# Optimization experiments

Measured on AMD Instinct MI355X. Metric: run time of the kernel, lower is better.

The kernel has to match this reference:

```python
import jax, jax.numpy as jnp
import numpy as np

S, B, E, H, V, L = 512, 64, 512, 768, 32000, 32
PAD_WORD, PAD_LABEL = 1, 0
PAD_BIAS = 10000.0


def _linear_init(key, fin, fout):
    # matches torch nn.Linear default U(-1/sqrt(fin), 1/sqrt(fin))
    kw, kb = jax.random.split(key)
    s = 1.0 / np.sqrt(fin)
    W = jax.random.uniform(kw, (fin, fout), minval=-s, maxval=s, dtype=jnp.float32)
    b = jax.random.uniform(kb, (fout,), minval=-s, maxval=s, dtype=jnp.float32)
    return W, b


def setup_inputs() -> dict:
    key = jax.random.key(0)
    ks = jax.random.split(key, 9)
    tokens = jax.random.randint(ks[0], (S, B), 0, V, dtype=jnp.int32)
    tags = jax.random.randint(ks[1], (S, B), 0, L, dtype=jnp.int32)
    embedding = jax.random.normal(ks[2], (V, E), dtype=jnp.float32)
    # gate order along the 4H axis: r, f, g, o (matches the 8 separate Linears, stacked)
    Wi_f, bi_f = _linear_init(ks[3], E, 4 * H)
    Wh_f, bh_f = _linear_init(ks[4], H, 4 * H)
    Wi_b, bi_b = _linear_init(ks[5], E, 4 * H)
    Wh_b, bh_b = _linear_init(ks[6], H, 4 * H)
    Wout, bout = _linear_init(ks[7], 2 * H, L)
    return {"tokens": tokens, "tags": tags, "embedding": embedding,
            "Wi_f": Wi_f, "bi_f": bi_f, "Wh_f": Wh_f, "bh_f": bh_f,
            "Wi_b": Wi_b, "bi_b": bi_b, "Wh_b": Wh_b, "bh_b": bh_b,
            "Wout": Wout, "bout": bout}


def _forward(tokens, embedding, Wi_f, bi_f, Wh_f, bh_f, Wi_b, bi_b, Wh_b, bh_b, Wout, bout):
    emb = embedding[tokens]                      # [S,B,E]
    b = tokens.shape[1]
    h = emb.shape[-1] * 0 + Wh_f.shape[0]
    # ---- forward direction: true LSTM-style recurrence ----
    xf = jnp.einsum('sbe,eg->sbg', emb, Wi_f) + bi_f   # [S,B,4H] precomputed input gates

    def step_f(carry, x):
        hid, c = carry
        g = x + hid @ Wh_f + bh_f
        r, f, gg, o = jnp.split(g, 4, axis=-1)
        c = jax.nn.sigmoid(f) * c + jax.nn.sigmoid(r) * jnp.tanh(gg)
        hid = jax.nn.sigmoid(o) * jnp.tanh(c)
        return (hid, c), hid

    z = jnp.zeros((b, h), dtype=emb.dtype)
    (hT, _), hs_f = jax.lax.scan(step_f, (z, z), xf)   # hs_f: [S,B,H]

    # ---- backward direction: source never updates `hidden`, so the hidden
    # projection uses the CONSTANT final forward hidden hT at every step.
    gb = jnp.einsum('sbe,eg->sbg', emb, Wi_b) + bi_b + hT @ Wh_b + bh_b  # [S,B,4H]
    r2, f2, g2, o2 = jnp.split(gb, 4, axis=-1)
    r2 = jax.nn.sigmoid(r2); f2 = jax.nn.sigmoid(f2)
    g2 = jnp.tanh(g2);       o2 = jax.nn.sigmoid(o2)

    def step_b(c2, gates):
        r, f, g, o = gates
        c2 = f * c2 + r * g
        return c2, o * jnp.tanh(c2)

    _, hs_b = jax.lax.scan(step_b, z, (r2, f2, g2, o2), reverse=True)  # [S,B,H], original order

    outputs = jnp.concatenate([hs_f, hs_b], axis=-1)   # [S,B,2H]
    out = outputs @ Wout + bout                        # [S,B,L]
    pad_mask = (tokens == PAD_WORD).astype(out.dtype)
    out = out.at[:, :, PAD_LABEL].add(pad_mask * PAD_BIAS)
    return out


def reference(tokens, tags, embedding, Wi_f, bi_f, Wh_f, bh_f, Wi_b, bi_b, Wh_b, bh_b, Wout, bout):
    del tags  # unused in forward, kept for signature fidelity
    return _forward(tokens, embedding, Wi_f, bi_f, Wh_f, bh_f, Wi_b, bi_b, Wh_b, bh_b, Wout, bout)
```

## Files before the change

kernel.cpp:

```cpp
#include <hip/hip_runtime.h>
#include <hip/hip_bf16.h>
#include <stdint.h>

typedef __attribute__((ext_vector_type(8))) short bf16x8;
typedef __attribute__((ext_vector_type(4))) float f32x4;
typedef __attribute__((ext_vector_type(4))) unsigned int u32x4;
typedef unsigned long long ull_t;

#define S_LEN 512
#define B_DIM 64
#define E_DIM 512
#define H_DIM 768
#define G4    3072
#define H2    1536
#define M_ROWS 32768
#define CHUNK 128
#define CM    8192
#define SLW   24
#define WPS   8
#define WPR   256
#define RWRD  4096
#define PSTR  16384
#define KRES  640
#define KREG  4
#define WROW  648

__device__ __forceinline__ float sigmf_(float x) { return 1.0f / (1.0f + __expf(-x)); }
__device__ __forceinline__ float tanhf2(float x) {
  x = fminf(fmaxf(x, -20.0f), 20.0f);
  float e = __expf(2.0f * x);
  return (e - 1.0f) / (e + 1.0f);
}
__device__ __forceinline__ float bfu(unsigned short u) { return __uint_as_float((unsigned)u << 16); }
__device__ __forceinline__ unsigned short packbf(float a) {
  __hip_bfloat16 t = __float2bfloat16(a);
  unsigned short b;
  __builtin_memcpy(&b, &t, 2);
  return b;
}

__global__ __launch_bounds__(256) void k_gather(const int* __restrict__ tokens,
                                                const float* __restrict__ emb,
                                                __hip_bfloat16* __restrict__ out) {
  const int t = blockIdx.x * 256 + threadIdx.x;
  const int e0 = t * 8;
  const int row = e0 >> 9;
  const int k = e0 & 511;
  const int tok = tokens[row];
  const float4* p = (const float4*)(emb + (size_t)tok * E_DIM + k);
  const float4 v0 = p[0], v1 = p[1];
  __align__(16) __hip_bfloat16 tmp[8];
  tmp[0] = __float2bfloat16(v0.x); tmp[1] = __float2bfloat16(v0.y);
  tmp[2] = __float2bfloat16(v0.z); tmp[3] = __float2bfloat16(v0.w);
  tmp[4] = __float2bfloat16(v1.x); tmp[5] = __float2bfloat16(v1.y);
  tmp[6] = __float2bfloat16(v1.z); tmp[7] = __float2bfloat16(v1.w);
  *(bf16x8*)(out + (size_t)t * 8) = *(const bf16x8*)tmp;
}

__global__ __launch_bounds__(256) void k_transpose_cast(const float* __restrict__ src,
                                                        __hip_bfloat16* __restrict__ dst,
                                                        int Rs, int Cs) {
  __shared__ float tile[32][33];
  const int tx = threadIdx.x & 31, ty = threadIdx.x >> 5;
  const int c0 = blockIdx.x * 32, r0 = blockIdx.y * 32;
  #pragma unroll
  for (int i = ty; i < 32; i += 8)
    tile[i][tx] = src[(size_t)(r0 + i) * Cs + c0 + tx];
  __syncthreads();
  #pragma unroll
  for (int i = ty; i < 32; i += 8)
    dst[(size_t)(c0 + i) * Rs + r0 + tx] = __float2bfloat16(tile[tx][i]);
}

__global__ __launch_bounds__(256) void k_bias(const float* __restrict__ bi,
                                              const float* __restrict__ bh,
                                              float* __restrict__ bias) {
  const int n = blockIdx.x * 256 + threadIdx.x;
  bias[n] = bi[n] + bh[n];
}

__global__ __launch_bounds__(256) void k_gemm_x(const __hip_bfloat16* __restrict__ A,
                                                const __hip_bfloat16* __restrict__ BT,
                                                const float* __restrict__ bias,
                                                __hip_bfloat16* __restrict__ C) {
  __shared__ __align__(16) __hip_bfloat16 As[128][40];
  __shared__ __align__(16) __hip_bfloat16 Bs[128][40];
  const int tid = threadIdx.x;
  const int wave = tid >> 6, lane = tid & 63;
  const int q = lane >> 4, lr = lane & 15;
  const int wm = (wave >> 1) * 64, wn = (wave & 1) * 64;
  const int m0 = blockIdx.y * 128, n0 = blockIdx.x * 128;
  const int srow = tid >> 2, skseg = (tid & 3) * 8;

  f32x4 acc[4][4];
  #pragma unroll
  for (int i = 0; i < 4; ++i)
    #pragma unroll
    for (int j = 0; j < 4; ++j) { f32x4 z = {0.f, 0.f, 0.f, 0.f}; acc[i][j] = z; }

  for (int kt = 0; kt < 16; ++kt) {
    __syncthreads();
    const int kbase = kt * 32 + skseg;
    *(bf16x8*)&As[srow][skseg]      = *(const bf16x8*)(A + (size_t)(m0 + srow) * E_DIM + kbase);
    *(bf16x8*)&As[srow + 64][skseg] = *(const bf16x8*)(A + (size_t)(m0 + srow + 64) * E_DIM + kbase);
    *(bf16x8*)&Bs[srow][skseg]      = *(const bf16x8*)(BT + (size_t)(n0 + srow) * E_DIM + kbase);
    *(bf16x8*)&Bs[srow + 64][skseg] = *(const bf16x8*)(BT + (size_t)(n0 + srow + 64) * E_DIM + kbase);
    __syncthreads();
    bf16x8 af[4], bfr[4];
    #pragma unroll
    for (int mt = 0; mt < 4; ++mt) af[mt] = *(const bf16x8*)&As[wm + mt * 16 + lr][q * 8];
    #pragma unroll
    for (int nt = 0; nt < 4; ++nt) bfr[nt] = *(const bf16x8*)&Bs[wn + nt * 16 + lr][q * 8];
    #pragma unroll
    for (int mt = 0; mt < 4; ++mt)
      #pragma unroll
      for (int nt = 0; nt < 4; ++nt)
        acc[mt][nt] = __builtin_amdgcn_mfma_f32_16x16x32_bf16(af[mt], bfr[nt], acc[mt][nt], 0, 0, 0);
  }
  #pragma unroll
  for (int mt = 0; mt < 4; ++mt) {
    #pragma unroll
    for (int nt = 0; nt < 4; ++nt) {
      const int col = n0 + wn + nt * 16 + lr;
      const float bv = bias[col];
      #pragma unroll
      for (int i = 0; i < 4; ++i) {
        const int row = m0 + wm + mt * 16 + q * 4 + i;
        C[(size_t)row * G4 + col] = __float2bfloat16(acc[mt][nt][i] + bv);
      }
    }
  }
}

__global__ __launch_bounds__(256, 1) void k_fwd_scan(const __hip_bfloat16* __restrict__ X,
                                                     const __hip_bfloat16* __restrict__ WhTf,
                                                     ull_t* __restrict__ hbuf,
                                                     __hip_bfloat16* __restrict__ Hs,
                                                     float* __restrict__ cstate,
                                                     float* __restrict__ hT,
                                                     int chunk) {
  const int bx = blockIdx.x;
  const int group = bx >> 5;
  const int slice = bx & 31;
  const int r0 = group * 16;
  const int j0 = slice * SLW;
  const int tid = threadIdx.x;
  const int w = tid >> 6;
  const int lane = tid & 63;
  const int q = lane >> 4, lr = lane & 15;
  const int base = chunk * CHUNK;

  const int prow = tid >> 4;
  const int pw   = tid & 15;

  const int row  = tid >> 3;
  const int wloc = tid & 7;
  const int col0 = 3 * wloc;

  __shared__ __align__(16) unsigned short wlds[4 * SLW * WROW];
  __shared__ __align__(16) unsigned short h_stage[16][776];
  __shared__ float g_lds[4][16][26];

  for (int c = tid; c < 96 * (KRES / 8); c += 256) {
    const int r = c / (KRES / 8), k8 = c % (KRES / 8);
    const int gate = r / SLW, n = r % SLW;
    const float4 v = *(const float4*)(WhTf + (size_t)(gate * H_DIM + j0 + n) * H_DIM + k8 * 8);
    *(float4*)(wlds + (size_t)r * WROW + k8 * 8) = v;
  }

  const int wn0 = lr;
  const int wn1 = 16 + (lr & 7);
  bf16x8 wr0[KREG], wr1[KREG];
  #pragma unroll
  for (int kk = 0; kk < KREG; ++kk) {
    const int ko = KRES + kk * 32 + q * 8;
    wr0[kk] = *(const bf16x8*)(WhTf + (size_t)(w * H_DIM + j0 + wn0) * H_DIM + ko);
    wr1[kk] = *(const bf16x8*)(WhTf + (size_t)(w * H_DIM + j0 + wn1) * H_DIM + ko);
  }

  float cr[3] = {0.f, 0.f, 0.f};
  if (tid < 128) {
    const float* cs = cstate + (size_t)(r0 + row) * H_DIM + j0 + col0;
    cr[0] = cs[0]; cr[1] = cs[1]; cr[2] = cs[2];
  }

  const unsigned skipbit = ((pw >> 2) == (slice & 3)) ? (1u << (slice >> 2)) : 0u;

  __syncthreads();

  for (int s = 0; s < CHUNK; ++s) {
    const int gs = base + s;

    unsigned short xs[4][3];
    if (tid < 128) {
      const unsigned short* xp = (const unsigned short*)(X + ((size_t)s * B_DIM + r0 + row) * G4 + j0 + col0);
      #pragma unroll
      for (int g = 0; g < 4; ++g)
        #pragma unroll
        for (int j = 0; j < 3; ++j) xs[g][j] = xp[g * H_DIM + j];
    }

    const ull_t* hc = hbuf + ((size_t)(gs & 1)) * PSTR + (size_t)group * RWRD
                    + (size_t)prow * WPR + 2 * pw;
    u32x4 d0 = {0,0,0,0}, d1 = {0,0,0,0}, d2 = {0,0,0,0}, d3 = {0,0,0,0};
    u32x4 d4 = {0,0,0,0}, d5 = {0,0,0,0}, d6 = {0,0,0,0}, d7 = {0,0,0,0};
    const unsigned pollmask = (s == 0) ? 0xFFu : (0xFFu ^ skipbit);
    {
      const unsigned e16 = (unsigned)(unsigned short)gs;
      unsigned need = pollmask;
      long guard = 0;
      for (;;) {
#define POLL_LD(i, dv) \
        if (need & (1u << (i))) \
          asm volatile("global_load_dwordx4 %0, %1, off sc0 sc1" \
                       : "=v"(dv) : "v"(hc + 32 * (i)) : "memory");
        POLL_LD(0, d0) POLL_LD(1, d1) POLL_LD(2, d2) POLL_LD(3, d3)
        POLL_LD(4, d4) POLL_LD(5, d5) POLL_LD(6, d6) POLL_LD(7, d7)
#undef POLL_LD
        asm volatile("s_waitcnt vmcnt(0)"
                     : "+v"(d0), "+v"(d1), "+v"(d2), "+v"(d3),
                       "+v"(d4), "+v"(d5), "+v"(d6), "+v"(d7)
                     :: "memory");
        unsigned nn = 0;
#define POLL_CK(i, dv) \
        if ((need & (1u << (i))) && \
            ((((dv).x & 0xFFFFu) != e16) || (((dv).z & 0xFFFFu) != e16))) nn |= 1u << (i);
        POLL_CK(0, d0) POLL_CK(1, d1) POLL_CK(2, d2) POLL_CK(3, d3)
        POLL_CK(4, d4) POLL_CK(5, d5) POLL_CK(6, d6) POLL_CK(7, d7)
#undef POLL_CK
        need = nn;
        if (!need) break;
        if (++guard > (1L << 20)) break;
        __builtin_amdgcn_s_sleep(1);
      }
    }
    {
#define STAGE_PAIR(i, dv) \
      if (pollmask & (1u << (i))) { \
        unsigned* hp = (unsigned*)&h_stage[prow][6 * pw + 96 * (i)]; \
        hp[0] = ((dv).x >> 16) | ((dv).y << 16); \
        hp[1] = ((dv).y >> 16) | ((dv).z & 0xFFFF0000u); \
        hp[2] = (dv).w; \
      }
      STAGE_PAIR(0, d0) STAGE_PAIR(1, d1) STAGE_PAIR(2, d2) STAGE_PAIR(3, d3)
      STAGE_PAIR(4, d4) STAGE_PAIR(5, d5) STAGE_PAIR(6, d6) STAGE_PAIR(7, d7)
#undef STAGE_PAIR
    }
    __syncthreads();

    f32x4 acc0 = {0.f, 0.f, 0.f, 0.f};
    f32x4 acc1 = {0.f, 0.f, 0.f, 0.f};
    {
      const unsigned short* wb = wlds + (size_t)w * SLW * WROW;
      #pragma unroll
      for (int kt = 0; kt < KRES / 32; ++kt) {
        const int ko = kt * 32 + q * 8;
        const bf16x8 a  = *(const bf16x8*)&h_stage[lr][ko];
        const bf16x8 b0 = *(const bf16x8*)(wb + (size_t)wn0 * WROW + ko);
        const bf16x8 b1 = *(const bf16x8*)(wb + (size_t)wn1 * WROW + ko);
        acc0 = __builtin_amdgcn_mfma_f32_16x16x32_bf16(a, b0, acc0, 0, 0, 0);
        acc1 = __builtin_amdgcn_mfma_f32_16x16x32_bf16(a, b1, acc1, 0, 0, 0);
      }
      #pragma unroll
      for (int kk = 0; kk < KREG; ++kk) {
        const bf16x8 a = *(const bf16x8*)&h_stage[lr][KRES + kk * 32 + q * 8];
        acc0 = __builtin_amdgcn_mfma_f32_16x16x32_bf16(a, wr0[kk], acc0, 0, 0, 0);
        acc1 = __builtin_amdgcn_mfma_f32_16x16x32_bf16(a, wr1[kk], acc1, 0, 0, 0);
      }
    }
    #pragma unroll
    for (int i = 0; i < 4; ++i) g_lds[w][q * 4 + i][lr] = acc0[i];
    if (lr < 8) {
      #pragma unroll
      for (int i = 0; i < 4; ++i) g_lds[w][q * 4 + i][16 + lr] = acc1[i];
    }
    __syncthreads();

    if (tid < 128) {
      float h[3];
      #pragma unroll
      for (int j = 0; j < 3; ++j) {
        const float rv = g_lds[0][row][col0 + j] + bfu(xs[0][j]);
        const float fv = g_lds[1][row][col0 + j] + bfu(xs[1][j]);
        const float gv = g_lds[2][row][col0 + j] + bfu(xs[2][j]);
        const float ov = g_lds[3][row][col0 + j] + bfu(xs[3][j]);
        const float c = sigmf_(fv) * cr[j] + sigmf_(rv) * tanhf2(gv);
        cr[j] = c;
        h[j] = sigmf_(ov) * tanhf2(c);
      }
      const unsigned short b0 = packbf(h[0]), b1 = packbf(h[1]), b2 = packbf(h[2]);
      const ull_t wv = (ull_t)(unsigned short)(gs + 1)
                     | ((ull_t)b0 << 16) | ((ull_t)b1 << 32) | ((ull_t)b2 << 48);
      __hip_atomic_store(hbuf + ((size_t)((gs + 1) & 1)) * PSTR + (size_t)group * RWRD
                         + (size_t)row * WPR + slice * WPS + wloc,
                         wv, __ATOMIC_RELAXED, __HIP_MEMORY_SCOPE_AGENT);
      h_stage[row][j0 + col0]     = b0;
      h_stage[row][j0 + col0 + 1] = b1;
      h_stage[row][j0 + col0 + 2] = b2;
      unsigned short* hsp = (unsigned short*)(Hs + ((size_t)gs * B_DIM + r0 + row) * H2 + j0 + col0);
      hsp[0] = b0; hsp[1] = b1; hsp[2] = b2;
      if (chunk == 3 && s == CHUNK - 1) {
        float* hp = hT + (size_t)(r0 + row) * H_DIM + j0 + col0;
        hp[0] = h[0]; hp[1] = h[1]; hp[2] = h[2];
      }
    }
  }

  if (tid < 128) {
    float* cs = cstate + (size_t)(r0 + row) * H_DIM + j0 + col0;
    cs[0] = cr[0]; cs[1] = cr[1]; cs[2] = cr[2];
  }
}

__global__ __launch_bounds__(256) void k_hTW(const float* __restrict__ hT,
                                             const float* __restrict__ Whb,
                                             float* __restrict__ hTW) {
  const int b = blockIdx.y;
  const int n = blockIdx.x * 256 + threadIdx.x;
  __shared__ float hs[768];
  for (int i = threadIdx.x; i < 768; i += 256) hs[i] = hT[b * 768 + i];
  __syncthreads();
  float acc = 0.f;
  #pragma unroll 4
  for (int k = 0; k < 768; ++k) acc += hs[k] * Whb[(size_t)k * G4 + n];
  hTW[(size_t)b * G4 + n] = acc;
}

__global__ __launch_bounds__(256) void k_bwd_scan(const __hip_bfloat16* __restrict__ X,
                                                  const float* __restrict__ hTW,
                                                  __hip_bfloat16* __restrict__ Hs,
                                                  float* __restrict__ c2state,
                                                  int chunk) {
  const int t = blockIdx.x * 256 + threadIdx.x;
  const int b = t / H_DIM;
  const int j = t % H_DIM;
  const int base = chunk * CHUNK;
  const float hw0 = hTW[(size_t)b * G4 + j];
  const float hw1 = hTW[(size_t)b * G4 + 768 + j];
  const float hw2 = hTW[(size_t)b * G4 + 1536 + j];
  const float hw3 = hTW[(size_t)b * G4 + 2304 + j];
  float c2 = c2state[t];
  for (int s = CHUNK - 1; s >= 0; --s) {
    const size_t xb = ((size_t)s * B_DIM + b) * G4 + j;
    const float r = sigmf_(__bfloat162float(X[xb]) + hw0);
    const float f = sigmf_(__bfloat162float(X[xb + 768]) + hw1);
    const float g = tanhf2(__bfloat162float(X[xb + 1536]) + hw2);
    const float o = sigmf_(__bfloat162float(X[xb + 2304]) + hw3);
    c2 = f * c2 + r * g;
    Hs[((size_t)(base + s) * B_DIM + b) * H2 + H_DIM + j] = __float2bfloat16(o * tanhf2(c2));
  }
  c2state[t] = c2;
}

__global__ __launch_bounds__(256) void k_out(const __hip_bfloat16* __restrict__ Hs,
                                             const float* __restrict__ Wout,
                                             const float* __restrict__ bout,
                                             const int* __restrict__ tokens,
                                             float* __restrict__ out) {
  __shared__ float rowbuf[8][1536];
  const int r0 = blockIdx.x * 8;
  const int tid = threadIdx.x;
  for (int idx = tid; idx < 8 * 1536; idx += 256) {
    const int rr = idx / 1536, k = idx % 1536;
    rowbuf[rr][k] = __bfloat162float(Hs[(size_t)(r0 + rr) * H2 + k]);
  }
  __syncthreads();
  const int l = tid & 31, rr = tid >> 5;
  float acc = bout[l];
  #pragma unroll 8
  for (int k = 0; k < 1536; ++k) acc += rowbuf[rr][k] * Wout[k * 32 + l];
  const int row = r0 + rr;
  if (l == 0 && tokens[row] == 1) acc += 10000.0f;
  out[(size_t)row * 32 + l] = acc;
}

extern "C" void kernel_launch(void* const* d_in, const int* in_sizes, int n_in,
                              void* d_out, int out_size, void* d_ws, size_t ws_size,
                              hipStream_t stream) {
  const int*   tokens = (const int*)d_in[0];
  const float* emb    = (const float*)d_in[2];
  const float* Wi_f   = (const float*)d_in[3];
  const float* bi_f   = (const float*)d_in[4];
  const float* Wh_f   = (const float*)d_in[5];
  const float* bh_f   = (const float*)d_in[6];
  const float* Wi_b   = (const float*)d_in[7];
  const float* bi_b   = (const float*)d_in[8];
  const float* Wh_b   = (const float*)d_in[9];
  const float* bh_b   = (const float*)d_in[10];
  const float* Wout   = (const float*)d_in[11];
  const float* bout   = (const float*)d_in[12];
  float* out = (float*)d_out;
  char* ws = (char*)d_ws;

  size_t off = 0;
  auto alloc = [&](size_t bytes) { size_t o = off; off += (bytes + 255) & ~(size_t)255; return o; };
  const size_t oHs    = alloc((size_t)M_ROWS * H2 * 2);
  const size_t oX     = alloc((size_t)CM * G4 * 2);
  const size_t oEmb   = alloc((size_t)M_ROWS * E_DIM * 2);
  const size_t oWiT   = alloc((size_t)G4 * E_DIM * 2);
  const size_t oWhTf  = alloc((size_t)G4 * H_DIM * 2);
  const size_t oBias  = alloc((size_t)G4 * 4);
  const size_t oHbuf  = alloc((size_t)2 * PSTR * 8);
  const size_t oCst   = alloc((size_t)B_DIM * H_DIM * 4);
  const size_t oHT    = alloc((size_t)B_DIM * H_DIM * 4);
  const size_t oHTW   = alloc((size_t)B_DIM * G4 * 4);
  const size_t oC2    = alloc((size_t)B_DIM * H_DIM * 4);
  (void)ws_size; (void)in_sizes; (void)n_in; (void)out_size;

  __hip_bfloat16* Hs   = (__hip_bfloat16*)(ws + oHs);
  __hip_bfloat16* X    = (__hip_bfloat16*)(ws + oX);
  __hip_bfloat16* Emb  = (__hip_bfloat16*)(ws + oEmb);
  __hip_bfloat16* WiT  = (__hip_bfloat16*)(ws + oWiT);
  __hip_bfloat16* WhTf = (__hip_bfloat16*)(ws + oWhTf);
  float*          Bias = (float*)(ws + oBias);
  ull_t*          Hbuf = (ull_t*)(ws + oHbuf);
  float*          Cst  = (float*)(ws + oCst);
  float*          HT   = (float*)(ws + oHT);
  float*          HTW  = (float*)(ws + oHTW);
  float*          C2   = (float*)(ws + oC2);

  hipMemsetAsync(ws + oHbuf, 0, (size_t)2 * PSTR * 8, stream);
  hipMemsetAsync(ws + oCst, 0, (size_t)B_DIM * H_DIM * 4, stream);
  hipMemsetAsync(ws + oC2, 0, (size_t)B_DIM * H_DIM * 4, stream);

  k_gather<<<8192, 256, 0, stream>>>(tokens, emb, Emb);
  k_transpose_cast<<<dim3(96, 24), 256, 0, stream>>>(Wh_f, WhTf, 768, 3072);

  k_transpose_cast<<<dim3(96, 16), 256, 0, stream>>>(Wi_f, WiT, 512, 3072);
  k_bias<<<12, 256, 0, stream>>>(bi_f, bh_f, Bias);
  for (int c = 0; c < 4; ++c) {
    k_gemm_x<<<dim3(24, 64), 256, 0, stream>>>(Emb + (size_t)c * CM * E_DIM, WiT, Bias, X);
    k_fwd_scan<<<128, 256, 0, stream>>>(X, WhTf, Hbuf, Hs, Cst, HT, c);
  }

  k_hTW<<<dim3(12, 64), 256, 0, stream>>>(HT, Wh_b, HTW);
  k_transpose_cast<<<dim3(96, 16), 256, 0, stream>>>(Wi_b, WiT, 512, 3072);
  k_bias<<<12, 256, 0, stream>>>(bi_b, bh_b, Bias);
  for (int c = 3; c >= 0; --c) {
    k_gemm_x<<<dim3(24, 64), 256, 0, stream>>>(Emb + (size_t)c * CM * E_DIM, WiT, Bias, X);
    k_bwd_scan<<<192, 256, 0, stream>>>(X, HTW, Hs, C2, c);
  }

  k_out<<<4096, 256, 0, stream>>>(Hs, Wout, bout, tokens, out);
}
```

Measured before the change: 3.187 ms.

## Overlap next-chunk input GEMM and output projection with recurrent scans

Extra blocks in the forward and backward scan kernels compute the next chunk's input-gate GEMM into a double-buffered X workspace while the scan blocks process the current chunk. The backward kernel also computes the output projection for already-finished chunks. The separate embedding gather kernel is removed by loading and casting embedding rows directly inside the GEMM tile loader. This hides GEMM and output time behind the latency-bound scans, at the cost of more workspace and possible contention with the scan blocks' synchronization and bandwidth.

```diff
diff --git a/kernel.cpp b/kernel.cpp
--- a/kernel.cpp
+++ b/kernel.cpp
@@ -24,6 +24,7 @@
 #define KRES  640
 #define KREG  4
 #define WROW  648
+#define NTILES 1536
 
 __device__ __forceinline__ float sigmf_(float x) { return 1.0f / (1.0f + __expf(-x)); }
 __device__ __forceinline__ float tanhf2(float x) {
@@ -37,24 +38,6 @@
   unsigned short b;
   __builtin_memcpy(&b, &t, 2);
   return b;
-}
-
-__global__ __launch_bounds__(256) void k_gather(const int* __restrict__ tokens,
-                                                const float* __restrict__ emb,
-                                                __hip_bfloat16* __restrict__ out) {
-  const int t = blockIdx.x * 256 + threadIdx.x;
-  const int e0 = t * 8;
-  const int row = e0 >> 9;
-  const int k = e0 & 511;
-  const int tok = tokens[row];
-  const float4* p = (const float4*)(emb + (size_t)tok * E_DIM + k);
-  const float4 v0 = p[0], v1 = p[1];
-  __align__(16) __hip_bfloat16 tmp[8];
-  tmp[0] = __float2bfloat16(v0.x); tmp[1] = __float2bfloat16(v0.y);
-  tmp[2] = __float2bfloat16(v0.z); tmp[3] = __float2bfloat16(v0.w);
-  tmp[4] = __float2bfloat16(v1.x); tmp[5] = __float2bfloat16(v1.y);
-  tmp[6] = __float2bfloat16(v1.z); tmp[7] = __float2bfloat16(v1.w);
-  *(bf16x8*)(out + (size_t)t * 8) = *(const bf16x8*)tmp;
 }
 
 __global__ __launch_bounds__(256) void k_transpose_cast(const float* __restrict__ src,
@@ -79,18 +62,23 @@
   bias[n] = bi[n] + bh[n];
 }
 
-__global__ __launch_bounds__(256) void k_gemm_x(const __hip_bfloat16* __restrict__ A,
-                                                const __hip_bfloat16* __restrict__ BT,
-                                                const float* __restrict__ bias,
-                                                __hip_bfloat16* __restrict__ C) {
-  __shared__ __align__(16) __hip_bfloat16 As[128][40];
-  __shared__ __align__(16) __hip_bfloat16 Bs[128][40];
+__device__ __forceinline__ void gemm_tile_g(char* pool, int tile,
+                                            const int* __restrict__ tokens_c,
+                                            const float* __restrict__ emb,
+                                            const __hip_bfloat16* __restrict__ BT,
+                                            const float* __restrict__ bias,
+                                            __hip_bfloat16* __restrict__ C) {
+  auto As = (__hip_bfloat16 (*)[40])pool;
+  auto Bs = (__hip_bfloat16 (*)[40])(pool + 10240);
   const int tid = threadIdx.x;
   const int wave = tid >> 6, lane = tid & 63;
   const int q = lane >> 4, lr = lane & 15;
   const int wm = (wave >> 1) * 64, wn = (wave & 1) * 64;
-  const int m0 = blockIdx.y * 128, n0 = blockIdx.x * 128;
+  const int nb = tile % 24, mb = tile / 24;
+  const int m0 = mb * 128, n0 = nb * 128;
   const int srow = tid >> 2, skseg = (tid & 3) * 8;
+  const int tok0 = tokens_c[m0 + srow];
+  const int tok1 = tokens_c[m0 + srow + 64];
 
   f32x4 acc[4][4];
   #pragma unroll
@@ -101,8 +89,26 @@
   for (int kt = 0; kt < 16; ++kt) {
     __syncthreads();
     const int kbase = kt * 32 + skseg;
-    *(bf16x8*)&As[srow][skseg]      = *(const bf16x8*)(A + (size_t)(m0 + srow) * E_DIM + kbase);
-    *(bf16x8*)&As[srow + 64][skseg] = *(const bf16x8*)(A + (size_t)(m0 + srow + 64) * E_DIM + kbase);
+    {
+      const float* ap = emb + (size_t)tok0 * E_DIM + kbase;
+      const float4 v0 = *(const float4*)ap, v1 = *(const float4*)(ap + 4);
+      __align__(16) __hip_bfloat16 t8[8];
+      t8[0] = __float2bfloat16(v0.x); t8[1] = __float2bfloat16(v0.y);
+      t8[2] = __float2bfloat16(v0.z); t8[3] = __float2bfloat16(v0.w);
+      t8[4] = __float2bfloat16(v1.x); t8[5] = __float2bfloat16(v1.y);
+      t8[6] = __float2bfloat16(v1.z); t8[7] = __float2bfloat16(v1.w);
+      *(bf16x8*)&As[srow][skseg] = *(const bf16x8*)t8;
+    }
+    {
+      const float* ap = emb + (size_t)tok1 * E_DIM + kbase;
+      const float4 v0 = *(const float4*)ap, v1 = *(const float4*)(ap + 4);
+      __align__(16) __hip_bfloat16 t8[8];
+      t8[0] = __float2bfloat16(v0.x); t8[1] = __float2bfloat16(v0.y);
+      t8[2] = __float2bfloat16(v0.z); t8[3] = __float2bfloat16(v0.w);
+      t8[4] = __float2bfloat16(v1.x); t8[5] = __float2bfloat16(v1.y);
+      t8[6] = __float2bfloat16(v1.z); t8[7] = __float2bfloat16(v1.w);
+      *(bf16x8*)&As[srow + 64][skseg] = *(const bf16x8*)t8;
+    }
     *(bf16x8*)&Bs[srow][skseg]      = *(const bf16x8*)(BT + (size_t)(n0 + srow) * E_DIM + kbase);
     *(bf16x8*)&Bs[srow + 64][skseg] = *(const bf16x8*)(BT + (size_t)(n0 + srow + 64) * E_DIM + kbase);
     __syncthreads();
@@ -132,14 +138,74 @@
   }
 }
 
-__global__ __launch_bounds__(256, 1) void k_fwd_scan(const __hip_bfloat16* __restrict__ X,
-                                                     const __hip_bfloat16* __restrict__ WhTf,
-                                                     ull_t* __restrict__ hbuf,
-                                                     __hip_bfloat16* __restrict__ Hs,
-                                                     float* __restrict__ cstate,
-                                                     float* __restrict__ hT,
-                                                     int chunk) {
+__global__ __launch_bounds__(256) void k_gemm_g(const int* __restrict__ tokens_c,
+                                                const float* __restrict__ emb,
+                                                const __hip_bfloat16* __restrict__ BT,
+                                                const float* __restrict__ bias,
+                                                __hip_bfloat16* __restrict__ C) {
+  __shared__ __align__(16) char pool[20480];
+  gemm_tile_g(pool, blockIdx.x, tokens_c, emb, BT, bias, C);
+}
+
+__device__ __forceinline__ void out_block8(char* pool, int ob,
+                                           const __hip_bfloat16* __restrict__ Hs,
+                                           const float* __restrict__ Wout,
+                                           const float* __restrict__ bout,
+                                           const int* __restrict__ tokens,
+                                           float* __restrict__ out) {
+  auto rowbuf = (float (*)[1536])pool;
+  const int r0 = ob * 8;
+  const int tid = threadIdx.x;
+  for (int idx = tid; idx < 8 * 1536; idx += 256) {
+    const int rr = idx / 1536, k = idx % 1536;
+    rowbuf[rr][k] = __bfloat162float(Hs[(size_t)(r0 + rr) * H2 + k]);
+  }
+  __syncthreads();
+  const int l = tid & 31, rr = tid >> 5;
+  float acc = bout[l];
+  #pragma unroll 8
+  for (int k = 0; k < 1536; ++k) acc += rowbuf[rr][k] * Wout[k * 32 + l];
+  const int row = r0 + rr;
+  if (l == 0 && tokens[row] == 1) acc += 10000.0f;
+  out[(size_t)row * 32 + l] = acc;
+  __syncthreads();
+}
+
+__global__ __launch_bounds__(256) void k_out(const __hip_bfloat16* __restrict__ Hs,
+                                             const float* __restrict__ Wout,
+                                             const float* __restrict__ bout,
+                                             const int* __restrict__ tokens,
+                                             float* __restrict__ out) {
+  __shared__ __align__(16) char pool[49152];
+  out_block8(pool, blockIdx.x, Hs, Wout, bout, tokens, out);
+}
+
+__global__ __launch_bounds__(256, 1) void k_fwd_fused(const __hip_bfloat16* __restrict__ X,
+                                                      const __hip_bfloat16* __restrict__ WhTf,
+                                                      ull_t* __restrict__ hbuf,
+                                                      __hip_bfloat16* __restrict__ Hs,
+                                                      float* __restrict__ cstate,
+                                                      float* __restrict__ hT,
+                                                      int chunk,
+                                                      const int* __restrict__ tokens_nx,
+                                                      const float* __restrict__ emb,
+                                                      const __hip_bfloat16* __restrict__ WiT_nx,
+                                                      const float* __restrict__ Bias_nx,
+                                                      __hip_bfloat16* __restrict__ Xw) {
+  __shared__ __align__(16) char pool[155904];
   const int bx = blockIdx.x;
+
+  if (bx >= 128) {
+    const int nw = gridDim.x - 128;
+    for (int t = bx - 128; t < NTILES; t += nw)
+      gemm_tile_g(pool, t, tokens_nx, emb, WiT_nx, Bias_nx, Xw);
+    return;
+  }
+
+  unsigned short* wlds = (unsigned short*)pool;
+  auto h_stage = (unsigned short (*)[776])(pool + 124416);
+  auto g_lds   = (float (*)[16][26])(pool + 149248);
+
   const int group = bx >> 5;
   const int slice = bx & 31;
   const int r0 = group * 16;
@@ -156,10 +222,6 @@
   const int row  = tid >> 3;
   const int wloc = tid & 7;
   const int col0 = 3 * wloc;
-
-  __shared__ __align__(16) unsigned short wlds[4 * SLW * WROW];
-  __shared__ __align__(16) unsigned short h_stage[16][776];
-  __shared__ float g_lds[4][16][26];
 
   for (int c = tid; c < 96 * (KRES / 8); c += 256) {
     const int r = c / (KRES / 8), k8 = c % (KRES / 8);
@@ -326,12 +388,38 @@
   hTW[(size_t)b * G4 + n] = acc;
 }
 
-__global__ __launch_bounds__(256) void k_bwd_scan(const __hip_bfloat16* __restrict__ X,
-                                                  const float* __restrict__ hTW,
-                                                  __hip_bfloat16* __restrict__ Hs,
-                                                  float* __restrict__ c2state,
-                                                  int chunk) {
-  const int t = blockIdx.x * 256 + threadIdx.x;
+__global__ __launch_bounds__(256) void k_bwd_fused(const __hip_bfloat16* __restrict__ X,
+                                                   const float* __restrict__ hTW,
+                                                   __hip_bfloat16* __restrict__ Hs,
+                                                   float* __restrict__ c2state,
+                                                   int chunk,
+                                                   const int* __restrict__ tokens_nx,
+                                                   const float* __restrict__ emb,
+                                                   const __hip_bfloat16* __restrict__ WiTb,
+                                                   const float* __restrict__ BiasB,
+                                                   __hip_bfloat16* __restrict__ Xw,
+                                                   int do_gemm, int out_chunk,
+                                                   const float* __restrict__ Wout,
+                                                   const float* __restrict__ bout,
+                                                   const int* __restrict__ tokens_all,
+                                                   float* __restrict__ out) {
+  __shared__ __align__(16) char pool[49152];
+  const int bx = blockIdx.x;
+
+  if (bx >= 320) {
+    if (out_chunk >= 0)
+      for (int ob = bx - 320; ob < 1024; ob += 128)
+        out_block8(pool, out_chunk * 1024 + ob, Hs, Wout, bout, tokens_all, out);
+    return;
+  }
+  if (bx >= 192) {
+    if (do_gemm)
+      for (int t = bx - 192; t < NTILES; t += 128)
+        gemm_tile_g(pool, t, tokens_nx, emb, WiTb, BiasB, Xw);
+    return;
+  }
+
+  const int t = bx * 256 + threadIdx.x;
   const int b = t / H_DIM;
   const int j = t % H_DIM;
   const int base = chunk * CHUNK;
@@ -350,28 +438,6 @@
     Hs[((size_t)(base + s) * B_DIM + b) * H2 + H_DIM + j] = __float2bfloat16(o * tanhf2(c2));
   }
   c2state[t] = c2;
-}
-
-__global__ __launch_bounds__(256) void k_out(const __hip_bfloat16* __restrict__ Hs,
-                                             const float* __restrict__ Wout,
-                                             const float* __restrict__ bout,
-                                             const int* __restrict__ tokens,
-                                             float* __restrict__ out) {
-  __shared__ float rowbuf[8][1536];
-  const int r0 = blockIdx.x * 8;
-  const int tid = threadIdx.x;
-  for (int idx = tid; idx < 8 * 1536; idx += 256) {
-    const int rr = idx / 1536, k = idx % 1536;
-    rowbuf[rr][k] = __bfloat162float(Hs[(size_t)(r0 + rr) * H2 + k]);
-  }
-  __syncthreads();
-  const int l = tid & 31, rr = tid >> 5;
-  float acc = bout[l];
-  #pragma unroll 8
-  for (int k = 0; k < 1536; ++k) acc += rowbuf[rr][k] * Wout[k * 32 + l];
-  const int row = r0 + rr;
-  if (l == 0 && tokens[row] == 1) acc += 10000.0f;
-  out[(size_t)row * 32 + l] = acc;
 }
 
 extern "C" void kernel_launch(void* const* d_in, const int* in_sizes, int n_in,
@@ -395,24 +461,29 @@
   size_t off = 0;
   auto alloc = [&](size_t bytes) { size_t o = off; off += (bytes + 255) & ~(size_t)255; return o; };
   const size_t oHs    = alloc((size_t)M_ROWS * H2 * 2);
-  const size_t oX     = alloc((size_t)CM * G4 * 2);
-  const size_t oEmb   = alloc((size_t)M_ROWS * E_DIM * 2);
-  const size_t oWiT   = alloc((size_t)G4 * E_DIM * 2);
+  const size_t oX0    = alloc((size_t)CM * G4 * 2);
   const size_t oWhTf  = alloc((size_t)G4 * H_DIM * 2);
-  const size_t oBias  = alloc((size_t)G4 * 4);
+  const size_t oWiTf  = alloc((size_t)G4 * E_DIM * 2);
+  const size_t oWiTb  = alloc((size_t)G4 * E_DIM * 2);
+  const size_t oBiasF = alloc((size_t)G4 * 4);
+  const size_t oBiasB = alloc((size_t)G4 * 4);
   const size_t oHbuf  = alloc((size_t)2 * PSTR * 8);
   const size_t oCst   = alloc((size_t)B_DIM * H_DIM * 4);
   const size_t oHT    = alloc((size_t)B_DIM * H_DIM * 4);
   const size_t oHTW   = alloc((size_t)B_DIM * G4 * 4);
   const size_t oC2    = alloc((size_t)B_DIM * H_DIM * 4);
-  (void)ws_size; (void)in_sizes; (void)n_in; (void)out_size;
+  const size_t oX1    = alloc((size_t)CM * G4 * 2);
+  const bool overlap = (off <= ws_size);
+  (void)in_sizes; (void)n_in; (void)out_size;
 
   __hip_bfloat16* Hs   = (__hip_bfloat16*)(ws + oHs);
-  __hip_bfloat16* X    = (__hip_bfloat16*)(ws + oX);
-  __hip_bfloat16* Emb  = (__hip_bfloat16*)(ws + oEmb);
-  __hip_bfloat16* WiT  = (__hip_bfloat16*)(ws + oWiT);
+  __hip_bfloat16* X0   = (__hip_bfloat16*)(ws + oX0);
+  __hip_bfloat16* X1   = overlap ? (__hip_bfloat16*)(ws + oX1) : X0;
   __hip_bfloat16* WhTf = (__hip_bfloat16*)(ws + oWhTf);
-  float*          Bias = (float*)(ws + oBias);
+  __hip_bfloat16* WiTf = (__hip_bfloat16*)(ws + oWiTf);
+  __hip_bfloat16* WiTb = (__hip_bfloat16*)(ws + oWiTb);
+  float*          BiasF= (float*)(ws + oBiasF);
+  float*          BiasB= (float*)(ws + oBiasB);
   ull_t*          Hbuf = (ull_t*)(ws + oHbuf);
   float*          Cst  = (float*)(ws + oCst);
   float*          HT   = (float*)(ws + oHT);
@@ -423,23 +494,49 @@
   hipMemsetAsync(ws + oCst, 0, (size_t)B_DIM * H_DIM * 4, stream);
   hipMemsetAsync(ws + oC2, 0, (size_t)B_DIM * H_DIM * 4, stream);
 
-  k_gather<<<8192, 256, 0, stream>>>(tokens, emb, Emb);
   k_transpose_cast<<<dim3(96, 24), 256, 0, stream>>>(Wh_f, WhTf, 768, 3072);
-
-  k_transpose_cast<<<dim3(96, 16), 256, 0, stream>>>(Wi_f, WiT, 512, 3072);
-  k_bias<<<12, 256, 0, stream>>>(bi_f, bh_f, Bias);
-  for (int c = 0; c < 4; ++c) {
-    k_gemm_x<<<dim3(24, 64), 256, 0, stream>>>(Emb + (size_t)c * CM * E_DIM, WiT, Bias, X);
-    k_fwd_scan<<<128, 256, 0, stream>>>(X, WhTf, Hbuf, Hs, Cst, HT, c);
-  }
-
-  k_hTW<<<dim3(12, 64), 256, 0, stream>>>(HT, Wh_b, HTW);
-  k_transpose_cast<<<dim3(96, 16), 256, 0, stream>>>(Wi_b, WiT, 512, 3072);
-  k_bias<<<12, 256, 0, stream>>>(bi_b, bh_b, Bias);
-  for (int c = 3; c >= 0; --c) {
-    k_gemm_x<<<dim3(24, 64), 256, 0, stream>>>(Emb + (size_t)c * CM * E_DIM, WiT, Bias, X);
-    k_bwd_scan<<<192, 256, 0, stream>>>(X, HTW, Hs, C2, c);
-  }
-
-  k_out<<<4096, 256, 0, stream>>>(Hs, Wout, bout, tokens, out);
-}
+  k_transpose_cast<<<dim3(96, 16), 256, 0, stream>>>(Wi_f, WiTf, 512, 3072);
+  k_transpose_cast<<<dim3(96, 16), 256, 0, stream>>>(Wi_b, WiTb, 512, 3072);
+  k_bias<<<12, 256, 0, stream>>>(bi_f, bh_f, BiasF);
+  k_bias<<<12, 256, 0, stream>>>(bi_b, bh_b, BiasB);
+
+  if (overlap) {
+    k_gemm_g<<<NTILES, 256, 0, stream>>>(tokens, emb, WiTf, BiasF, X0);
+    k_fwd_fused<<<240, 256, 0, stream>>>(X0, WhTf, Hbuf, Hs, Cst, HT, 0,
+                                         tokens + 1 * CM, emb, WiTf, BiasF, X1);
+    k_fwd_fused<<<240, 256, 0, stream>>>(X1, WhTf, Hbuf, Hs, Cst, HT, 1,
+                                         tokens + 2 * CM, emb, WiTf, BiasF, X0);
+    k_fwd_fused<<<240, 256, 0, stream>>>(X0, WhTf, Hbuf, Hs, Cst, HT, 2,
+                                         tokens + 3 * CM, emb, WiTf, BiasF, X1);
+    k_fwd_fused<<<240, 256, 0, stream>>>(X1, WhTf, Hbuf, Hs, Cst, HT, 3,
+                                         tokens + 3 * CM, emb, WiTb, BiasB, X0);
+    k_hTW<<<dim3(12, 64), 256, 0, stream>>>(HT, Wh_b, HTW);
+    k_bwd_fused<<<448, 256, 0, stream>>>(X0, HTW, Hs, C2, 3,
+                                         tokens + 2 * CM, emb, WiTb, BiasB, X1, 1, -1,
+                                         Wout, bout, tokens, out);
+    k_bwd_fused<<<448, 256, 0, stream>>>(X1, HTW, Hs, C2, 2,
+                                         tokens + 1 * CM, emb, WiTb, BiasB, X0, 1, 3,
+                                         Wout, bout, tokens, out);
+    k_bwd_fused<<<448, 256, 0, stream>>>(X0, HTW, Hs, C2, 1,
+                                         tokens + 0 * CM, emb, WiTb, BiasB, X1, 1, 2,
+                                         Wout, bout, tokens, out);
+    k_bwd_fused<<<448, 256, 0, stream>>>(X1, HTW, Hs, C2, 0,
+                                         tokens, emb, WiTb, BiasB, X0, 0, 1,
+                                         Wout, bout, tokens, out);
+    k_out<<<1024, 256, 0, stream>>>(Hs, Wout, bout, tokens, out);
+  } else {
+    for (int c = 0; c < 4; ++c) {
+      k_gemm_g<<<NTILES, 256, 0, stream>>>(tokens + (size_t)c * CM, emb, WiTf, BiasF, X0);
+      k_fwd_fused<<<128, 256, 0, stream>>>(X0, WhTf, Hbuf, Hs, Cst, HT, c,
+                                           tokens, emb, WiTf, BiasF, X0);
+    }
+    k_hTW<<<dim3(12, 64), 256, 0, stream>>>(HT, Wh_b, HTW);
+    for (int c = 3; c >= 0; --c) {
+      k_gemm_g<<<NTILES, 256, 0, stream>>>(tokens + (size_t)c * CM, emb, WiTb, BiasB, X0);
+      k_bwd_fused<<<192, 256, 0, stream>>>(X0, HTW, Hs, C2, c,
+                                           tokens, emb, WiTb, BiasB, X0, 0, -1,
+                                           Wout, bout, tokens, out);
+    }
+    k_out<<<4096, 256, 0, stream>>>(Hs, Wout, bout, tokens, out);
+  }
+}
```

Result: slower. 3.603 ms (+13.1%).
